# Kernel tuning notes

Hardware: AMD Instinct MI355X
Metric: run time of the kernel (lower is better)

The kernel has to match this reference:

```python
import jax, jax.numpy as jnp
import numpy as np

# ---- constants from the source module ----
NB = [[0,1,2,3],[0,1,4],[0,2,5],[0,3,6],[1,4,7],[2,5,8],[3,6,9],[4,7,10],[5,8,11],[6,9],[7,10],[8,11],[12,13,14,15],[12,13,16],[12,14,17],[12,15],[13,16,18],[14,17,19],[16,18,20],[17,19,21],[18,20,22],[19,21,23],[20,22],[21,23]]
PARENT = np.array([0,0,0,0,1,2,3,4,5,6,7,8,9,9,9,12,13,14,16,17,18,19,20,21])  # root parent sentinel handled separately
KJ, NV, PREG = 24, 6890, 200
LEN = np.array([len(n) for n in NB])
NBR_IDX = np.zeros((KJ,4), np.int32)
NBR_VALID = np.zeros((KJ,4), np.float32)
for k, n in enumerate(NB):
    NBR_IDX[k,:len(n)] = n; NBR_VALID[k,:len(n)] = 1.0
BETA_POS = np.zeros((KJ,17), np.float32); BETA_POS[np.arange(KJ), 4*LEN] = 1.0
SLICE_MASK = np.zeros((23,17), np.float32)
for j in range(23):
    SLICE_MASK[j,:4*LEN[j]+1] = 1.0  # self.K[j] has 4*len(NB[j])+1 rows
NBR_IDX = jnp.asarray(NBR_IDX); NBR_VALID = jnp.asarray(NBR_VALID)
BETA_POS = jnp.asarray(BETA_POS); SLICE_MASK = jnpp = jnp.asarray(SLICE_MASK)


def setup_inputs() -> dict:
    key = jax.random.key(0)
    ks = jax.random.split(key, 9)
    V = jax.random.normal(ks[0], (PREG, NV, 3), jnp.float32)
    T = jax.random.normal(ks[1], (PREG, NV, 3), jnp.float32)
    J = jax.random.normal(ks[2], (PREG, KJ, 3), jnp.float32)
    theta = 0.3 * jax.random.normal(ks[3], (PREG, 72), jnp.float32)
    W_prime = jax.random.uniform(ks[4], (NV, KJ), jnp.float32)
    W_i = jax.random.uniform(ks[5], (NV, KJ), jnp.float32)
    W_i = W_i / W_i.sum(axis=1, keepdims=True)
    A = jax.random.uniform(ks[6], (23, NV), jnp.float32)
    K_mats = 0.01 * jax.random.normal(ks[7], (23, 17, 3 * NV), jnp.float32)
    K_mats = K_mats * SLICE_MASK[:, :, None]  # zero rows beyond the ragged per-joint size
    beta_2 = jnp.ones((1,), jnp.float32)
    return {"V": V, "T": T, "J": J, "theta": theta, "W_prime": W_prime, "W_i": W_i, "A": A, "K_mats": K_mats, "beta_2": beta_2, "epoch": 1}


def _rodrigues(pose):  # pose: (K,3)
    angle = jnp.maximum(jnp.linalg.norm(pose, axis=1, keepdims=True), 1e-8)
    axis = pose / angle
    x, y, z = axis[:, 0], axis[:, 1], axis[:, 2]
    zero = jnp.zeros_like(x)
    skew = jnp.stack([zero, -z, y, z, zero, -x, -y, x, zero], axis=1).reshape(-1, 3, 3)
    outer = axis[:, :, None] * axis[:, None, :]
    c = jnp.cos(angle)[:, :, None]
    s = jnp.sin(angle)[:, :, None]
    eye = jnp.eye(3, dtype=pose.dtype)[None]
    return c * eye + (1.0 - c) * outer + s * skew


def _compute_G(pose72, Jp):  # pose72: (72,), Jp: (K,3) -> (K,4,4)
    R = _rodrigues(pose72.reshape(KJ, 3))
    t = Jp - jnp.concatenate([jnp.zeros((1, 3), Jp.dtype), Jp[PARENT[1:]]], axis=0)
    G_local = jnp.zeros((KJ, 4, 4), Jp.dtype)
    G_local = G_local.at[:, :3, :3].set(R).at[:, :3, 3].set(t).at[:, 3, 3].set(1.0)
    Gs = [G_local[0]]
    for i in range(1, KJ):  # fixed 24-joint kinematic tree
        Gs.append(Gs[PARENT[i]] @ G_local[i])
    G = jnp.stack(Gs, axis=0)
    off = jnp.einsum('kij,kj->ki', G[:, :3, :3], Jp)  # homogeneous w=0 -> rotation only
    return G.at[:, :3, 3].add(-off)


def _axis2quat(p):  # (M,3) -> (M,4)
    angle = jnp.sqrt(jnp.maximum(jnp.sum(p ** 2, axis=1), 1e-16))
    n = p / angle[:, None]
    s = jnp.sin(angle / 2)
    return jnp.stack([n[:, 0] * s, n[:, 1] * s, n[:, 2] * s, jnp.cos(angle / 2) - 1.0], axis=1)


def reference(V, T, J, theta, W_prime, W_i, A, K_mats, beta_2, epoch):
    P = V.shape[0]
    b2 = beta_2[0]
    # normalized skinning weights
    W_relu = jax.nn.relu(W_prime)
    W_change = W_relu / (W_relu.sum(axis=1, keepdims=True) + 1e-8)
    # per-pose global joint transforms
    G_prime = jax.vmap(_compute_G)(theta, J)  # (P,K,4,4)
    # quaternion features and blend-shape correction
    q = _axis2quat(theta.reshape(P * KJ, 3)).reshape(P, KJ, 4)
    qg = q[:, NBR_IDX, :] * NBR_VALID[None, :, :, None]       # (P,K,4,4) neighbor gather
    q17 = jnp.concatenate([qg.reshape(P, KJ, 16), jnp.zeros((P, KJ, 1), q.dtype)], axis=-1)
    q17 = q17 + BETA_POS[None] * b2                            # beta_2 at column 4*len
    qm = q17[:, 1:, :] * SLICE_MASK[None]                      # ragged slice q_ne[:, j+1, :lenK]
    contrib = jnp.einsum('pjl,jlm->pjm', qm, K_mats).reshape(P, 23, NV, 3)
    T_p = jnp.einsum('pjnc,jn->pnc', contrib, jax.nn.relu(A)) + T
    # linear blend skinning
    T_h = jnp.concatenate([T_p, jnp.ones((P, NV, 1), T_p.dtype)], axis=-1)
    transformed = jnp.einsum('pkij,pnj->pnki', G_prime[:, :, :3, :], T_h)  # (P,N,K,3)
    verts = jnp.einsum('nk,pnkc->pnc', W_change, transformed)
    # energies
    e = float(epoch)
    g_wi = 0.1 * np.exp(-0.1 * e)
    g_w = 0.002 * np.exp(-0.008 * e)
    g_a = 0.001 * np.exp(-0.008 * e)
    g_k = 0.1 * np.exp(-0.008 * e)
    E_D = jnp.sum((V - verts) ** 2)
    E_Wi = jnp.sum((W_change - W_i) ** 2)
    E_W = jnp.sum(jnp.abs(W_change))
    E_A = jnp.sum(jnp.abs(A))
    E_K = jnp.sum(jnp.sqrt(jnp.sum(K_mats ** 2, axis=(1, 2))))
    E = E_D + g_wi * E_Wi + g_w * E_W + g_a * E_A + g_k * E_K
    return (E, verts)
```

## Files before the change

kernel.cpp:

```cpp
#include <hip/hip_runtime.h>
#include <math.h>

#define KJ 24
#define NV 6890
#define PREG 200
#define M_TOT (NV*3)
#define KDIM 391
#define KPAD 416
#define TP_STRIDE 20672
#define NMT64 323
#define NKB (NMT64*2)

#define EDP_OFF 0
#define EKP_OFF 5400
#define WIP_OFF 101984
#define EWP_OFF 102016
#define EAP_OFF 102048
#define RED_OFF 102080
#define G_OFF   102112
#define TPH_OFF_U  319424
#define TP2H_OFF_U 4453824
#define QBH_OFF_U 10903488
#define QBL_OFF_U 11009984

typedef __attribute__((ext_vector_type(8))) short short8;
typedef __attribute__((ext_vector_type(4))) float f32x4;
typedef __attribute__((ext_vector_type(4))) unsigned int u32x4;

__constant__ int c_PARENT[24] = {0,0,0,0,1,2,3,4,5,6,7,8,9,9,9,12,13,14,16,17,18,19,20,21};
__constant__ int c_DEPTH[24]  = {0,1,1,1,2,2,2,3,3,3,4,4,4,4,4,5,5,5,6,6,7,7,8,8};
__constant__ int c_LEN[24]    = {4,3,3,3,3,3,3,3,3,2,2,2,4,3,3,2,3,3,3,3,3,3,2,2};
__constant__ int c_NBR[24][4] = {
  {0,1,2,3},{0,1,4,0},{0,2,5,0},{0,3,6,0},{1,4,7,0},{2,5,8,0},{3,6,9,0},{4,7,10,0},
  {5,8,11,0},{6,9,0,0},{7,10,0,0},{8,11,0,0},{12,13,14,15},{12,13,16,0},{12,14,17,0},
  {12,15,0,0},{13,16,18,0},{14,17,19,0},{16,18,20,0},{17,19,21,0},{18,20,22,0},
  {19,21,23,0},{20,22,0,0},{21,23,0,0}};

__device__ __forceinline__ float waveReduce(float v) {
  #pragma unroll
  for (int off = 32; off > 0; off >>= 1) v += __shfl_down(v, off, 64);
  return v;
}
__device__ __forceinline__ unsigned short f2bf(float x) {
  union { float f; unsigned u; } v; v.f = x;
  unsigned r = v.u + 0x7FFFu + ((v.u >> 16) & 1u);
  return (unsigned short)(r >> 16);
}
__device__ __forceinline__ float bf2f(unsigned short h) {
  union { unsigned u; float f; } v; v.u = ((unsigned)h) << 16; return v.f;
}

__global__ __launch_bounds__(256) void kPre(const float* __restrict__ J,
                                            const float* __restrict__ theta,
                                            const float* __restrict__ beta2,
                                            const float* __restrict__ Wp,
                                            const float* __restrict__ Wi,
                                            const float* __restrict__ A,
                                            float* __restrict__ ws) {
  unsigned short* qbh = (unsigned short*)ws + QBH_OFF_U;
  unsigned short* qbl = (unsigned short*)ws + QBL_OFF_U;
  int b = blockIdx.x;
  if (b < 50) {
    __shared__ float Gl[4][24][12];
    __shared__ float Gg[4][24][12];
    __shared__ float q[4][24][4];
    int w = threadIdx.x >> 6, t = threadIdx.x & 63;
    int p = b*4 + w;
    if (t < 24) {
      float x = theta[p*72 + 3*t + 0];
      float y = theta[p*72 + 3*t + 1];
      float z = theta[p*72 + 3*t + 2];
      float n2 = x*x + y*y + z*z;
      float ang = fmaxf(sqrtf(n2), 1e-8f);
      float ia = 1.f/ang;
      float ax = x*ia, ay = y*ia, az = z*ia;
      float c = cosf(ang), s = sinf(ang), C = 1.f - c;
      float jx = J[p*72+3*t], jy = J[p*72+3*t+1], jz = J[p*72+3*t+2];
      float tx = jx, ty = jy, tz = jz;
      if (t > 0) {
        int par = c_PARENT[t];
        tx -= J[p*72+3*par]; ty -= J[p*72+3*par+1]; tz -= J[p*72+3*par+2];
      }
      Gl[w][t][0]=c+C*ax*ax;   Gl[w][t][1]=C*ax*ay-s*az; Gl[w][t][2]=C*ax*az+s*ay; Gl[w][t][3]=tx;
      Gl[w][t][4]=C*ax*ay+s*az;Gl[w][t][5]=c+C*ay*ay;    Gl[w][t][6]=C*ay*az-s*ax; Gl[w][t][7]=ty;
      Gl[w][t][8]=C*ax*az-s*ay;Gl[w][t][9]=C*ay*az+s*ax; Gl[w][t][10]=c+C*az*az;   Gl[w][t][11]=tz;
      float ang2 = sqrtf(fmaxf(n2, 1e-16f));
      float inv2 = 1.f/ang2;
      float s2 = sinf(0.5f*ang2);
      q[w][t][0] = x*inv2*s2; q[w][t][1] = y*inv2*s2; q[w][t][2] = z*inv2*s2;
      q[w][t][3] = cosf(0.5f*ang2) - 1.f;
    }
    __syncthreads();
    for (int lev = 0; lev <= 8; lev++) {
      if (t < 24 && c_DEPTH[t] == lev) {
        if (lev == 0) {
          for (int i2 = 0; i2 < 12; i2++) Gg[w][0][i2] = Gl[w][0][i2];
        } else {
          int par = c_PARENT[t];
          for (int r = 0; r < 3; r++) {
            float g0 = Gg[w][par][r*4+0], g1 = Gg[w][par][r*4+1];
            float g2 = Gg[w][par][r*4+2], g3 = Gg[w][par][r*4+3];
            for (int c2 = 0; c2 < 4; c2++) {
              float v = g0*Gl[w][t][0+c2] + g1*Gl[w][t][4+c2] + g2*Gl[w][t][8+c2];
              if (c2 == 3) v += g3;
              Gg[w][t][r*4+c2] = v;
            }
          }
        }
      }
      __syncthreads();
    }
    if (t < 24) {
      float jx = J[p*72+3*t], jy = J[p*72+3*t+1], jz = J[p*72+3*t+2];
      float* gp = ws + G_OFF + p*288 + t*12;
      #pragma unroll
      for (int r = 0; r < 3; r++) {
        float off = Gg[w][t][r*4+0]*jx + Gg[w][t][r*4+1]*jy + Gg[w][t][r*4+2]*jz;
        Gg[w][t][r*4+3] -= off;
      }
      #pragma unroll
      for (int i2 = 0; i2 < 12; i2++) gp[i2] = Gg[w][t][i2];
    }
    __syncthreads();
    float b2 = beta2[0];
    for (int e = t; e < KDIM; e += 64) {
      int j = e / 17, l = e - 17*j;
      int k = j + 1;
      float val = 0.f;
      if (l < 4*c_LEN[j] + 1) {
        if (l < 16) {
          int sidx = l >> 2, cc = l & 3;
          if (sidx < c_LEN[k]) val = q[w][c_NBR[k][sidx]][cc];
        }
        if (l == 4*c_LEN[k]) val += b2;
      }
      unsigned short hi = f2bf(val);
      unsigned short lo = f2bf(val - bf2f(hi));
      qbh[p*KPAD + e] = hi;
      qbl[p*KPAD + e] = lo;
    }
    for (int e = KDIM + t; e < KPAD; e += 64) {
      qbh[p*KPAD + e] = 0; qbl[p*KPAD + e] = 0;
    }
  } else {
    int d = b - 50;
    int t = threadIdx.x;
    int n = d*256 + t;
    float ewi = 0.f, ew = 0.f, ea = 0.f;
    if (n < NV) {
      float wv[24]; float sum = 0.f;
      const float4* wp4 = (const float4*)(Wp + n*24);
      #pragma unroll
      for (int i = 0; i < 6; i++) {
        float4 v4 = wp4[i];
        wv[4*i+0] = fmaxf(v4.x, 0.f); wv[4*i+1] = fmaxf(v4.y, 0.f);
        wv[4*i+2] = fmaxf(v4.z, 0.f); wv[4*i+3] = fmaxf(v4.w, 0.f);
        sum += wv[4*i+0]+wv[4*i+1]+wv[4*i+2]+wv[4*i+3];
      }
      float inv = 1.f/(sum + 1e-8f);
      #pragma unroll
      for (int k = 0; k < 24; k++) {
        float wc = wv[k]*inv;
        ew += fabsf(wc);
        float dd = wc - Wi[n*24+k];
        ewi += dd*dd;
      }
    }
    for (int i = d*256 + t; i < 23*NV; i += 27*256) ea += fabsf(A[i]);
    for (int i = d*256 + t; i < 56*KPAD; i += 27*256) {
      qbh[200*KPAD + i] = 0; qbl[200*KPAD + i] = 0;
    }
    __shared__ float red[3][4];
    int lane = t & 63, wv2 = t >> 6;
    ewi = waveReduce(ewi); ew = waveReduce(ew); ea = waveReduce(ea);
    if (lane == 0) { red[0][wv2] = ewi; red[1][wv2] = ew; red[2][wv2] = ea; }
    __syncthreads();
    if (t == 0) {
      ws[WIP_OFF + d] = red[0][0]+red[0][1]+red[0][2]+red[0][3];
      ws[EWP_OFF + d] = red[1][0]+red[1][1]+red[1][2]+red[1][3];
      ws[EAP_OFF + d] = red[2][0]+red[2][1]+red[2][2]+red[2][3];
    }
  }
}

template<int KS0, int NKS, int JMIN>
__device__ __forceinline__ void kb_body(const float* __restrict__ A,
                                        const float* __restrict__ K,
                                        const unsigned short* __restrict__ qbh,
                                        const unsigned short* __restrict__ qbl,
                                        float* __restrict__ Sk,
                                        short (*__restrict__ SBh)[64*32],
                                        short (*__restrict__ SBl)[64*32],
                                        float (*__restrict__ SA)[24],
                                        float* __restrict__ ek,
                                        float* __restrict__ ws,
                                        unsigned short* __restrict__ TPd,
                                        int m0, int flat) {
  const int tid = threadIdx.x;
  const int w = tid >> 6, lane = tid & 63;
  const int r = lane & 15, qd = lane >> 4;
  const int krow = tid >> 3, mseg = (tid & 7) * 8;
  const int mm = m0 + mseg;
  const int nb0 = m0 / 3;
  const int mrow2 = tid >> 2, kq2 = tid & 3;
  const int swr = ((mrow2 >> 4)*64 + kq2*16 + (mrow2 & 15)) * 8;

  if (tid < 23) ek[tid] = 0.f;
  for (int i = tid; i < 14*24; i += 256) {
    int jj = i / 24, nn = i - jj*24;
    int j2 = JMIN + jj, n2 = nb0 + nn;
    ((float*)SA)[i] = (j2 < 23 && n2 < NV) ? fmaxf(A[j2*NV + n2], 0.f) : 0.f;
  }

  f32x4 acc[4][4];
  #pragma unroll
  for (int h = 0; h < 4; h++)
    #pragma unroll
    for (int f = 0; f < 4; f++) acc[h][f] = (f32x4){0.f,0.f,0.f,0.f};

  int aofs[4];
  #pragma unroll
  for (int h = 0; h < 4; h++) aofs[h] = (w*64 + h*16 + r)*KPAD + KS0*32 + qd*8;

  short8 ah[2][4], al[2][4];
  float kv[8];

  auto loadK = [&](int ks) {
    int kg = (KS0 + ks)*32 + krow;
    #pragma unroll
    for (int i = 0; i < 8; i++) kv[i] = 0.f;
    if (kg < KDIM) {
      const float* kr = K + (size_t)kg*M_TOT + mm;
      if (mm + 7 < M_TOT) {
        float4 a4 = *(const float4*)kr; float4 b4 = *(const float4*)(kr+4);
        kv[0]=a4.x; kv[1]=a4.y; kv[2]=a4.z; kv[3]=a4.w;
        kv[4]=b4.x; kv[5]=b4.y; kv[6]=b4.z; kv[7]=b4.w;
      } else {
        #pragma unroll
        for (int i = 0; i < 8; i++) if (mm+i < M_TOT) kv[i] = kr[i];
      }
    }
  };
  auto stageK = [&](int ks) {
    int kg = (KS0 + ks)*32 + krow;
    float wv[8]; float sq = 0.f;
    #pragma unroll
    for (int i = 0; i < 8; i++) wv[i] = 0.f;
    if (kg < KDIM) {
      int jj = kg/17 - JMIN;
      int nb = mm / 3;
      float av[4];
      #pragma unroll
      for (int i = 0; i < 4; i++) av[i] = SA[jj][nb - nb0 + i];
      #pragma unroll
      for (int i = 0; i < 8; i++) {
        float a = (mm+i < M_TOT) ? av[(mm+i)/3 - nb] : 0.f;
        wv[i] = kv[i]*a;
        sq = fmaf(kv[i], kv[i], sq);
      }
    }
    #pragma unroll
    for (int c = 0; c < 4; c++)
      *(float2*)&Sk[krow*66 + mseg + 2*c] = make_float2(wv[2*c], wv[2*c+1]);
    sq += __shfl_xor(sq, 1, 64);
    sq += __shfl_xor(sq, 2, 64);
    sq += __shfl_xor(sq, 4, 64);
    if ((tid & 7) == 0 && kg < KDIM) atomicAdd(&ek[kg/17], sq);
  };
  auto xpose = [&](int buf) {
    float vv[8];
    #pragma unroll
    for (int j = 0; j < 8; j++) vv[j] = Sk[(kq2*8 + j)*66 + mrow2];
    unsigned dh[4], dl[4];
    #pragma unroll
    for (int c = 0; c < 4; c++) {
      unsigned short h0 = f2bf(vv[2*c]),   h1 = f2bf(vv[2*c+1]);
      unsigned short l0 = f2bf(vv[2*c]   - bf2f(h0));
      unsigned short l1 = f2bf(vv[2*c+1] - bf2f(h1));
      dh[c] = (unsigned)h0 | ((unsigned)h1 << 16);
      dl[c] = (unsigned)l0 | ((unsigned)l1 << 16);
    }
    *(u32x4*)&SBh[buf][swr] = (u32x4){dh[0], dh[1], dh[2], dh[3]};
    *(u32x4*)&SBl[buf][swr] = (u32x4){dl[0], dl[1], dl[2], dl[3]};
  };

  loadK(0);
  #pragma unroll
  for (int h = 0; h < 4; h++) {
    ah[0][h] = *(const short8*)(qbh + aofs[h]);
    al[0][h] = *(const short8*)(qbl + aofs[h]);
  }
  stageK(0);
  __syncthreads();
  xpose(0);
  #pragma unroll
  for (int h = 0; h < 4; h++) {
    ah[1][h] = *(const short8*)(qbh + aofs[h] + 32);
    al[1][h] = *(const short8*)(qbl + aofs[h] + 32);
  }
  __syncthreads();

  #pragma unroll
  for (int ks = 0; ks < NKS; ks++) {
    const int cur = ks & 1, nxt = cur ^ 1;
    if (ks + 1 < NKS) loadK(ks + 1);
    short8 bfh[4], bfl[4];
    #pragma unroll
    for (int f = 0; f < 4; f++) {
      bfh[f] = *(const short8*)&SBh[cur][(f*64 + lane)*8];
      bfl[f] = *(const short8*)&SBl[cur][(f*64 + lane)*8];
    }
    #pragma unroll
    for (int f = 0; f < 4; f++)
      #pragma unroll
      for (int h = 0; h < 4; h++) {
        acc[h][f] = __builtin_amdgcn_mfma_f32_16x16x32_bf16(ah[cur][h], bfh[f], acc[h][f], 0, 0, 0);
        acc[h][f] = __builtin_amdgcn_mfma_f32_16x16x32_bf16(ah[cur][h], bfl[f], acc[h][f], 0, 0, 0);
        acc[h][f] = __builtin_amdgcn_mfma_f32_16x16x32_bf16(al[cur][h], bfh[f], acc[h][f], 0, 0, 0);
      }
    if (ks + 1 < NKS) stageK(ks + 1);
    if (ks + 2 < NKS) {
      const int o = (ks + 2) * 32;
      #pragma unroll
      for (int h = 0; h < 4; h++) {
        ah[cur][h] = *(const short8*)(qbh + aofs[h] + o);
        al[cur][h] = *(const short8*)(qbl + aofs[h] + o);
      }
    }
    __syncthreads();
    if (ks + 1 < NKS) xpose(nxt);
    __syncthreads();
  }

  if (tid < 23) ws[EKP_OFF + tid*NKB + flat] = ek[tid];
  #pragma unroll
  for (int h = 0; h < 4; h++)
    #pragma unroll
    for (int f = 0; f < 4; f++)
      #pragma unroll
      for (int g = 0; g < 4; g++) {
        int p = w*64 + h*16 + qd*4 + g;
        if (p < PREG)
          TPd[(size_t)p*TP_STRIDE + m0 + f*16 + r] = f2bf(acc[h][f][g]);
      }
}

__global__ __launch_bounds__(256) void kB(const float* __restrict__ A,
                                          const float* __restrict__ K,
                                          float* __restrict__ ws) {
  __shared__ float Sk[32*66];
  __shared__ short SBh[2][64*32];
  __shared__ short SBl[2][64*32];
  __shared__ float SA[14][24];
  __shared__ float ek[23];
  const unsigned short* qbh = (const unsigned short*)ws + QBH_OFF_U;
  const unsigned short* qbl = (const unsigned short*)ws + QBL_OFF_U;
  unsigned short* tph  = (unsigned short*)ws + TPH_OFF_U;
  unsigned short* tp2h = (unsigned short*)ws + TP2H_OFF_U;
  const int m0 = blockIdx.x * 64;
  const int flat = blockIdx.x + blockIdx.y * NMT64;
  if (blockIdx.y == 0)
    kb_body<0, 7, 0>(A, K, qbh, qbl, Sk, SBh, SBl, SA, ek, ws, tph,  m0, flat);
  else
    kb_body<7, 6, 13>(A, K, qbh, qbl, Sk, SBh, SBl, SA, ek, ws, tp2h, m0, flat);
}

__global__ __launch_bounds__(256) void kC(const float* __restrict__ V,
                                          const float* __restrict__ T,
                                          const float* __restrict__ Wp,
                                          const float* __restrict__ ws,
                                          float* __restrict__ out) {
  int p0 = blockIdx.y * 8;
  int n = blockIdx.x*256 + threadIdx.x;
  const unsigned short* tph  = (const unsigned short*)ws + TPH_OFF_U;
  const unsigned short* tp2h = (const unsigned short*)ws + TP2H_OFF_U;
  __shared__ float tmp[4];
  float ed = 0.f;
  if (n < NV) {
    float wv[24]; float sum = 0.f;
    const float4* wp4 = (const float4*)(Wp + n*24);
    #pragma unroll
    for (int i = 0; i < 6; i++) {
      float4 v4 = wp4[i];
      wv[4*i+0] = fmaxf(v4.x, 0.f); wv[4*i+1] = fmaxf(v4.y, 0.f);
      wv[4*i+2] = fmaxf(v4.z, 0.f); wv[4*i+3] = fmaxf(v4.w, 0.f);
      sum += wv[4*i+0]+wv[4*i+1]+wv[4*i+2]+wv[4*i+3];
    }
    float inv = 1.f/(sum + 1e-8f);
    for (int pp = 0; pp < 8; pp++) {
      int p = p0 + pp;
      const float* __restrict__ gp = ws + G_OFF + (size_t)p*288;
      float M[12];
      #pragma unroll
      for (int i = 0; i < 12; i++) M[i] = 0.f;
      #pragma unroll
      for (int k = 0; k < 24; k++) {
        float wc = wv[k];
        #pragma unroll
        for (int i = 0; i < 12; i++)
          M[i] = fmaf(wc, gp[k*12 + i], M[i]);
      }
      #pragma unroll
      for (int i = 0; i < 12; i++) M[i] *= inv;
      size_t tb = (size_t)p*M_TOT + 3*n;
      size_t pb = (size_t)p*TP_STRIDE + 3*n;
      float t0 = bf2f(tph[pb + 0]) + bf2f(tp2h[pb + 0]) + T[tb + 0];
      float t1 = bf2f(tph[pb + 1]) + bf2f(tp2h[pb + 1]) + T[tb + 1];
      float t2 = bf2f(tph[pb + 2]) + bf2f(tp2h[pb + 2]) + T[tb + 2];
      float v0 = M[0]*t0 + M[1]*t1 + M[2]*t2  + M[3];
      float v1 = M[4]*t0 + M[5]*t1 + M[6]*t2  + M[7];
      float v2 = M[8]*t0 + M[9]*t1 + M[10]*t2 + M[11];
      out[1+tb+0] = v0; out[1+tb+1] = v1; out[1+tb+2] = v2;
      float d0 = V[tb+0]-v0, d1 = V[tb+1]-v1, d2 = V[tb+2]-v2;
      ed += d0*d0 + d1*d1 + d2*d2;
    }
  }
  ed = waveReduce(ed);
  int lane = threadIdx.x & 63, w = threadIdx.x >> 6;
  if (lane == 0) tmp[w] = ed;
  __syncthreads();
  if (threadIdx.x == 0)
    ((float*)ws)[EDP_OFF + blockIdx.y*27 + blockIdx.x] = tmp[0]+tmp[1]+tmp[2]+tmp[3];
}

__global__ __launch_bounds__(256) void kF1(float* __restrict__ ws) {
  __shared__ float sb[4];
  int b = blockIdx.x, t = threadIdx.x, lane = t & 63, w = t >> 6;
  if (b < 23) {
    float s = 0.f;
    for (int i = t; i < NKB; i += 256) s += ws[EKP_OFF + b*NKB + i];
    s = waveReduce(s);
    if (lane == 0) sb[w] = s;
    __syncthreads();
    if (t == 0) ws[RED_OFF + b] = sb[0]+sb[1]+sb[2]+sb[3];
  } else if (b == 23) {
    float s = 0.f;
    for (int i = t; i < 675; i += 256) s += ws[EDP_OFF + i];
    s = waveReduce(s);
    if (lane == 0) sb[w] = s;
    __syncthreads();
    if (t == 0) ws[RED_OFF + 23] = sb[0]+sb[1]+sb[2]+sb[3];
  } else {
    if (w == 0) {
      float s = (lane < 27) ? ws[WIP_OFF + lane] : 0.f;
      s = waveReduce(s);
      if (lane == 0) ws[RED_OFF + 24] = s;
    } else if (w == 1) {
      float s = (lane < 27) ? ws[EWP_OFF + lane] : 0.f;
      s = waveReduce(s);
      if (lane == 0) ws[RED_OFF + 25] = s;
    } else if (w == 2) {
      float s = (lane < 27) ? ws[EAP_OFF + lane] : 0.f;
      s = waveReduce(s);
      if (lane == 0) ws[RED_OFF + 26] = s;
    }
  }
}

__global__ void kF2(const int* __restrict__ epoch, const float* __restrict__ ws,
                    float* __restrict__ out) {
  int t = threadIdx.x;
  float s = (t < 23) ? sqrtf(ws[RED_OFF + t]) : 0.f;
  s = waveReduce(s);
  if (t == 0) {
    float e    = (float)epoch[0];
    float g_wi = 0.1f   * expf(-0.1f  * e);
    float g_w  = 0.002f * expf(-0.008f* e);
    float g_a  = 0.001f * expf(-0.008f* e);
    float g_k  = 0.1f   * expf(-0.008f* e);
    out[0] = ws[RED_OFF+23] + g_wi*ws[RED_OFF+24] + g_w*ws[RED_OFF+25]
           + g_a*ws[RED_OFF+26] + g_k*s;
  }
}

extern "C" void kernel_launch(void* const* d_in, const int* in_sizes, int n_in,
                              void* d_out, int out_size, void* d_ws, size_t ws_size,
                              hipStream_t stream) {
  const float* V     = (const float*)d_in[0];
  const float* T     = (const float*)d_in[1];
  const float* J     = (const float*)d_in[2];
  const float* theta = (const float*)d_in[3];
  const float* Wp    = (const float*)d_in[4];
  const float* Wi    = (const float*)d_in[5];
  const float* A     = (const float*)d_in[6];
  const float* K     = (const float*)d_in[7];
  const float* b2    = (const float*)d_in[8];
  const int*   epoch = (const int*)d_in[9];
  float* out = (float*)d_out;
  float* ws  = (float*)d_ws;

  hipLaunchKernelGGL(kPre, dim3(77),        dim3(256), 0, stream,
                     J, theta, b2, Wp, Wi, A, ws);
  hipLaunchKernelGGL(kB,   dim3(NMT64, 2),  dim3(256), 0, stream, A, K, ws);
  hipLaunchKernelGGL(kC,   dim3(27, 25),    dim3(256), 0, stream, V, T, Wp, ws, out);
  hipLaunchKernelGGL(kF1,  dim3(25),        dim3(256), 0, stream, ws);
  hipLaunchKernelGGL(kF2,  dim3(1),         dim3(64),  0, stream, epoch, ws, out);
}
```

Measured before the change: 177.5 us.

## Deepen K-tile software pipeline in kB and drop LDS atomics for E_K

```diff
diff --git a/kernel.cpp b/kernel.cpp
--- a/kernel.cpp
+++ b/kernel.cpp
@@ -188,11 +188,11 @@
                                         const float* __restrict__ K,
                                         const unsigned short* __restrict__ qbh,
                                         const unsigned short* __restrict__ qbl,
-                                        float* __restrict__ Sk,
+                                        float (*__restrict__ Sk)[32*66],
                                         short (*__restrict__ SBh)[64*32],
                                         short (*__restrict__ SBl)[64*32],
                                         float (*__restrict__ SA)[24],
-                                        float* __restrict__ ek,
+                                        float* __restrict__ ek2,
                                         float* __restrict__ ws,
                                         unsigned short* __restrict__ TPd,
                                         int m0, int flat) {
@@ -205,7 +205,6 @@
   const int mrow2 = tid >> 2, kq2 = tid & 3;
   const int swr = ((mrow2 >> 4)*64 + kq2*16 + (mrow2 & 15)) * 8;
 
-  if (tid < 23) ek[tid] = 0.f;
   for (int i = tid; i < 14*24; i += 256) {
     int jj = i / 24, nn = i - jj*24;
     int j2 = JMIN + jj, n2 = nb0 + nn;
@@ -223,76 +222,74 @@
   for (int h = 0; h < 4; h++) aofs[h] = (w*64 + h*16 + r)*KPAD + KS0*32 + qd*8;
 
   short8 ah[2][4], al[2][4];
-  float kv[8];
-
-  auto loadK = [&](int ks) {
-    int kg = (KS0 + ks)*32 + krow;
-    #pragma unroll
-    for (int i = 0; i < 8; i++) kv[i] = 0.f;
-    if (kg < KDIM) {
-      const float* kr = K + (size_t)kg*M_TOT + mm;
-      if (mm + 7 < M_TOT) {
-        float4 a4 = *(const float4*)kr; float4 b4 = *(const float4*)(kr+4);
-        kv[0]=a4.x; kv[1]=a4.y; kv[2]=a4.z; kv[3]=a4.w;
-        kv[4]=b4.x; kv[5]=b4.y; kv[6]=b4.z; kv[7]=b4.w;
-      } else {
-        #pragma unroll
-        for (int i = 0; i < 8; i++) if (mm+i < M_TOT) kv[i] = kr[i];
-      }
-    }
-  };
-  auto stageK = [&](int ks) {
-    int kg = (KS0 + ks)*32 + krow;
-    float wv[8]; float sq = 0.f;
-    #pragma unroll
-    for (int i = 0; i < 8; i++) wv[i] = 0.f;
-    if (kg < KDIM) {
-      int jj = kg/17 - JMIN;
-      int nb = mm / 3;
-      float av[4];
-      #pragma unroll
-      for (int i = 0; i < 4; i++) av[i] = SA[jj][nb - nb0 + i];
-      #pragma unroll
-      for (int i = 0; i < 8; i++) {
-        float a = (mm+i < M_TOT) ? av[(mm+i)/3 - nb] : 0.f;
-        wv[i] = kv[i]*a;
-        sq = fmaf(kv[i], kv[i], sq);
-      }
-    }
-    #pragma unroll
-    for (int c = 0; c < 4; c++)
-      *(float2*)&Sk[krow*66 + mseg + 2*c] = make_float2(wv[2*c], wv[2*c+1]);
-    sq += __shfl_xor(sq, 1, 64);
-    sq += __shfl_xor(sq, 2, 64);
-    sq += __shfl_xor(sq, 4, 64);
-    if ((tid & 7) == 0 && kg < KDIM) atomicAdd(&ek[kg/17], sq);
-  };
-  auto xpose = [&](int buf) {
-    float vv[8];
-    #pragma unroll
-    for (int j = 0; j < 8; j++) vv[j] = Sk[(kq2*8 + j)*66 + mrow2];
-    unsigned dh[4], dl[4];
-    #pragma unroll
-    for (int c = 0; c < 4; c++) {
-      unsigned short h0 = f2bf(vv[2*c]),   h1 = f2bf(vv[2*c+1]);
-      unsigned short l0 = f2bf(vv[2*c]   - bf2f(h0));
-      unsigned short l1 = f2bf(vv[2*c+1] - bf2f(h1));
-      dh[c] = (unsigned)h0 | ((unsigned)h1 << 16);
-      dl[c] = (unsigned)l0 | ((unsigned)l1 << 16);
-    }
-    *(u32x4*)&SBh[buf][swr] = (u32x4){dh[0], dh[1], dh[2], dh[3]};
-    *(u32x4*)&SBl[buf][swr] = (u32x4){dl[0], dl[1], dl[2], dl[3]};
-  };
-
-  loadK(0);
+  float kvA[8], kvB[8];
+
+#define LOADK(KSV, KV) do {                                                    \
+    int kg_ = (KS0 + (KSV))*32 + krow;                                         \
+    for (int i_ = 0; i_ < 8; i_++) KV[i_] = 0.f;                               \
+    if (kg_ < KDIM) {                                                          \
+      const float* kr_ = K + (size_t)kg_*M_TOT + mm;                           \
+      if (mm + 7 < M_TOT) {                                                    \
+        float4 a4_ = *(const float4*)kr_; float4 b4_ = *(const float4*)(kr_+4);\
+        KV[0]=a4_.x; KV[1]=a4_.y; KV[2]=a4_.z; KV[3]=a4_.w;                    \
+        KV[4]=b4_.x; KV[5]=b4_.y; KV[6]=b4_.z; KV[7]=b4_.w;                    \
+      } else {                                                                 \
+        for (int i_ = 0; i_ < 8; i_++) if (mm+i_ < M_TOT) KV[i_] = kr_[i_];    \
+      }                                                                        \
+    } } while (0)
+
+#define STAGEK(KSV, KV) do {                                                   \
+    int kg_ = (KS0 + (KSV))*32 + krow;                                         \
+    float wv_[8]; float sq_ = 0.f;                                             \
+    for (int i_ = 0; i_ < 8; i_++) wv_[i_] = 0.f;                              \
+    if (kg_ < KDIM) {                                                          \
+      int jj_ = kg_/17 - JMIN;                                                 \
+      int nb_ = mm / 3;                                                        \
+      float av_[4];                                                            \
+      for (int i_ = 0; i_ < 4; i_++) av_[i_] = SA[jj_][nb_ - nb0 + i_];        \
+      for (int i_ = 0; i_ < 8; i_++) {                                         \
+        float a_ = (mm+i_ < M_TOT) ? av_[(mm+i_)/3 - nb_] : 0.f;               \
+        wv_[i_] = KV[i_]*a_;                                                   \
+        sq_ = fmaf(KV[i_], KV[i_], sq_);                                       \
+      }                                                                        \
+    }                                                                          \
+    for (int c_ = 0; c_ < 4; c_++)                                             \
+      *(float2*)&Sk[(KSV)&1][krow*66 + mseg + 2*c_] =                          \
+        make_float2(wv_[2*c_], wv_[2*c_+1]);                                   \
+    sq_ += __shfl_xor(sq_, 1, 64);                                             \
+    sq_ += __shfl_xor(sq_, 2, 64);                                             \
+    sq_ += __shfl_xor(sq_, 4, 64);                                             \
+    if ((tid & 7) == 0) ek2[(KSV)*32 + krow] = sq_;                            \
+  } while (0)
+
+#define XPOSE(KSV) do {                                                        \
+    float vv_[8];                                                              \
+    for (int j_ = 0; j_ < 8; j_++)                                             \
+      vv_[j_] = Sk[(KSV)&1][(kq2*8 + j_)*66 + mrow2];                          \
+    unsigned dh_[4], dl_[4];                                                   \
+    for (int c_ = 0; c_ < 4; c_++) {                                           \
+      unsigned short h0_ = f2bf(vv_[2*c_]),   h1_ = f2bf(vv_[2*c_+1]);         \
+      unsigned short l0_ = f2bf(vv_[2*c_]   - bf2f(h0_));                      \
+      unsigned short l1_ = f2bf(vv_[2*c_+1] - bf2f(h1_));                      \
+      dh_[c_] = (unsigned)h0_ | ((unsigned)h1_ << 16);                         \
+      dl_[c_] = (unsigned)l0_ | ((unsigned)l1_ << 16);                         \
+    }                                                                          \
+    *(u32x4*)&SBh[(KSV)&1][swr] = (u32x4){dh_[0], dh_[1], dh_[2], dh_[3]};     \
+    *(u32x4*)&SBl[(KSV)&1][swr] = (u32x4){dl_[0], dl_[1], dl_[2], dl_[3]};     \
+  } while (0)
+
+  LOADK(0, kvA);
   #pragma unroll
   for (int h = 0; h < 4; h++) {
     ah[0][h] = *(const short8*)(qbh + aofs[h]);
     al[0][h] = *(const short8*)(qbl + aofs[h]);
   }
-  stageK(0);
+  STAGEK(0, kvA);
+  LOADK(1, kvB);
   __syncthreads();
-  xpose(0);
+  XPOSE(0);
+  STAGEK(1, kvB);
+  LOADK(2, kvA);
   #pragma unroll
   for (int h = 0; h < 4; h++) {
     ah[1][h] = *(const short8*)(qbh + aofs[h] + 32);
@@ -302,8 +299,10 @@
 
   #pragma unroll
   for (int ks = 0; ks < NKS; ks++) {
-    const int cur = ks & 1, nxt = cur ^ 1;
-    if (ks + 1 < NKS) loadK(ks + 1);
+    const int cur = ks & 1;
+    if (ks + 3 < NKS) {
+      if (cur == 1) LOADK(ks + 3, kvA); else LOADK(ks + 3, kvB);
+    }
     short8 bfh[4], bfl[4];
     #pragma unroll
     for (int f = 0; f < 4; f++) {
@@ -318,7 +317,6 @@
         acc[h][f] = __builtin_amdgcn_mfma_f32_16x16x32_bf16(ah[cur][h], bfl[f], acc[h][f], 0, 0, 0);
         acc[h][f] = __builtin_amdgcn_mfma_f32_16x16x32_bf16(al[cur][h], bfh[f], acc[h][f], 0, 0, 0);
       }
-    if (ks + 1 < NKS) stageK(ks + 1);
     if (ks + 2 < NKS) {
       const int o = (ks + 2) * 32;
       #pragma unroll
@@ -327,12 +325,24 @@
         al[cur][h] = *(const short8*)(qbl + aofs[h] + o);
       }
     }
+    if (ks + 2 < NKS) {
+      if (cur == 0) STAGEK(ks + 2, kvA); else STAGEK(ks + 2, kvB);
+    }
+    if (ks + 1 < NKS) XPOSE(ks + 1);
     __syncthreads();
-    if (ks + 1 < NKS) xpose(nxt);
-    __syncthreads();
-  }
-
-  if (tid < 23) ws[EKP_OFF + tid*NKB + flat] = ek[tid];
+  }
+#undef LOADK
+#undef STAGEK
+#undef XPOSE
+
+  if (tid < 23) {
+    float s = 0.f;
+    for (int i2 = 0; i2 < NKS*32; i2++) {
+      int kg = KS0*32 + i2;
+      if (kg < KDIM && kg/17 == tid) s += ek2[i2];
+    }
+    ws[EKP_OFF + tid*NKB + flat] = s;
+  }
   #pragma unroll
   for (int h = 0; h < 4; h++)
     #pragma unroll
@@ -348,11 +358,11 @@
 __global__ __launch_bounds__(256) void kB(const float* __restrict__ A,
                                           const float* __restrict__ K,
                                           float* __restrict__ ws) {
-  __shared__ float Sk[32*66];
+  __shared__ float Sk[2][32*66];
   __shared__ short SBh[2][64*32];
   __shared__ short SBl[2][64*32];
   __shared__ float SA[14][24];
-  __shared__ float ek[23];
+  __shared__ float ek2[7*32];
   const unsigned short* qbh = (const unsigned short*)ws + QBH_OFF_U;
   const unsigned short* qbl = (const unsigned short*)ws + QBL_OFF_U;
   unsigned short* tph  = (unsigned short*)ws + TPH_OFF_U;
@@ -360,9 +370,9 @@
   const int m0 = blockIdx.x * 64;
   const int flat = blockIdx.x + blockIdx.y * NMT64;
   if (blockIdx.y == 0)
-    kb_body<0, 7, 0>(A, K, qbh, qbl, Sk, SBh, SBl, SA, ek, ws, tph,  m0, flat);
+    kb_body<0, 7, 0>(A, K, qbh, qbl, Sk, SBh, SBl, SA, ek2, ws, tph,  m0, flat);
   else
-    kb_body<7, 6, 13>(A, K, qbh, qbl, Sk, SBh, SBl, SA, ek, ws, tp2h, m0, flat);
+    kb_body<7, 6, 13>(A, K, qbh, qbl, Sk, SBh, SBl, SA, ek2, ws, tp2h, m0, flat);
 }
 
 __global__ __launch_bounds__(256) void kC(const float* __restrict__ V,
```

Measured after the change: 186.3 us. +5.0%, slower.

## Split K-projection GEMM four ways and move K-norm energy into prologue

Applied to the files above, without the earlier changes.

```diff
diff --git a/kernel.cpp b/kernel.cpp
--- a/kernel.cpp
+++ b/kernel.cpp
@@ -9,7 +9,6 @@
 #define KPAD 416
 #define TP_STRIDE 20672
 #define NMT64 323
-#define NKB (NMT64*2)
 
 #define EDP_OFF 0
 #define EKP_OFF 5400
@@ -18,10 +17,13 @@
 #define EAP_OFF 102048
 #define RED_OFF 102080
 #define G_OFF   102112
+#define TPQ_U   4134400
 #define TPH_OFF_U  319424
-#define TP2H_OFF_U 4453824
-#define QBH_OFF_U 10903488
-#define QBL_OFF_U 11009984
+#define TP2H_OFF_U (TPH_OFF_U + TPQ_U)
+#define TP3H_OFF_U (TPH_OFF_U + 2*TPQ_U)
+#define TP4H_OFF_U (TPH_OFF_U + 3*TPQ_U)
+#define QBH_OFF_U  16857024
+#define QBL_OFF_U  16963520
 
 typedef __attribute__((ext_vector_type(8))) short short8;
 typedef __attribute__((ext_vector_type(4))) float f32x4;
@@ -56,6 +58,7 @@
                                             const float* __restrict__ Wp,
                                             const float* __restrict__ Wi,
                                             const float* __restrict__ A,
+                                            const float* __restrict__ K,
                                             float* __restrict__ ws) {
   unsigned short* qbh = (unsigned short*)ws + QBH_OFF_U;
   unsigned short* qbl = (unsigned short*)ws + QBL_OFF_U;
@@ -142,7 +145,7 @@
     for (int e = KDIM + t; e < KPAD; e += 64) {
       qbh[p*KPAD + e] = 0; qbl[p*KPAD + e] = 0;
     }
-  } else {
+  } else if (b < 77) {
     int d = b - 50;
     int t = threadIdx.x;
     int n = d*256 + t;
@@ -180,6 +183,18 @@
       ws[EWP_OFF + d] = red[1][0]+red[1][1]+red[1][2]+red[1][3];
       ws[EAP_OFF + d] = red[2][0]+red[2][1]+red[2][2]+red[2][3];
     }
+  } else {
+    int kg = b - 77;
+    int t = threadIdx.x;
+    const float* kr = K + (size_t)kg*M_TOT;
+    float s = 0.f;
+    for (int i = t; i < M_TOT; i += 256) { float v = kr[i]; s = fmaf(v, v, s); }
+    __shared__ float sb[4];
+    int lane = t & 63, w = t >> 6;
+    s = waveReduce(s);
+    if (lane == 0) sb[w] = s;
+    __syncthreads();
+    if (t == 0) ws[EKP_OFF + kg] = sb[0]+sb[1]+sb[2]+sb[3];
   }
 }
 
@@ -192,10 +207,8 @@
                                         short (*__restrict__ SBh)[64*32],
                                         short (*__restrict__ SBl)[64*32],
                                         float (*__restrict__ SA)[24],
-                                        float* __restrict__ ek,
-                                        float* __restrict__ ws,
                                         unsigned short* __restrict__ TPd,
-                                        int m0, int flat) {
+                                        int m0) {
   const int tid = threadIdx.x;
   const int w = tid >> 6, lane = tid & 63;
   const int r = lane & 15, qd = lane >> 4;
@@ -205,7 +218,6 @@
   const int mrow2 = tid >> 2, kq2 = tid & 3;
   const int swr = ((mrow2 >> 4)*64 + kq2*16 + (mrow2 & 15)) * 8;
 
-  if (tid < 23) ek[tid] = 0.f;
   for (int i = tid; i < 14*24; i += 256) {
     int jj = i / 24, nn = i - jj*24;
     int j2 = JMIN + jj, n2 = nb0 + nn;
@@ -243,7 +255,7 @@
   };
   auto stageK = [&](int ks) {
     int kg = (KS0 + ks)*32 + krow;
-    float wv[8]; float sq = 0.f;
+    float wv[8];
     #pragma unroll
     for (int i = 0; i < 8; i++) wv[i] = 0.f;
     if (kg < KDIM) {
@@ -256,16 +268,11 @@
       for (int i = 0; i < 8; i++) {
         float a = (mm+i < M_TOT) ? av[(mm+i)/3 - nb] : 0.f;
         wv[i] = kv[i]*a;
-        sq = fmaf(kv[i], kv[i], sq);
       }
     }
     #pragma unroll
     for (int c = 0; c < 4; c++)
       *(float2*)&Sk[krow*66 + mseg + 2*c] = make_float2(wv[2*c], wv[2*c+1]);
-    sq += __shfl_xor(sq, 1, 64);
-    sq += __shfl_xor(sq, 2, 64);
-    sq += __shfl_xor(sq, 4, 64);
-    if ((tid & 7) == 0 && kg < KDIM) atomicAdd(&ek[kg/17], sq);
   };
   auto xpose = [&](int buf) {
     float vv[8];
@@ -332,7 +339,6 @@
     __syncthreads();
   }
 
-  if (tid < 23) ws[EKP_OFF + tid*NKB + flat] = ek[tid];
   #pragma unroll
   for (int h = 0; h < 4; h++)
     #pragma unroll
@@ -352,17 +358,17 @@
   __shared__ short SBh[2][64*32];
   __shared__ short SBl[2][64*32];
   __shared__ float SA[14][24];
-  __shared__ float ek[23];
   const unsigned short* qbh = (const unsigned short*)ws + QBH_OFF_U;
   const unsigned short* qbl = (const unsigned short*)ws + QBL_OFF_U;
-  unsigned short* tph  = (unsigned short*)ws + TPH_OFF_U;
-  unsigned short* tp2h = (unsigned short*)ws + TP2H_OFF_U;
   const int m0 = blockIdx.x * 64;
-  const int flat = blockIdx.x + blockIdx.y * NMT64;
   if (blockIdx.y == 0)
-    kb_body<0, 7, 0>(A, K, qbh, qbl, Sk, SBh, SBl, SA, ek, ws, tph,  m0, flat);
+    kb_body<0, 4, 0>(A, K, qbh, qbl, Sk, SBh, SBl, SA, (unsigned short*)ws + TPH_OFF_U,  m0);
+  else if (blockIdx.y == 1)
+    kb_body<4, 3, 7>(A, K, qbh, qbl, Sk, SBh, SBl, SA, (unsigned short*)ws + TP2H_OFF_U, m0);
+  else if (blockIdx.y == 2)
+    kb_body<7, 3, 13>(A, K, qbh, qbl, Sk, SBh, SBl, SA, (unsigned short*)ws + TP3H_OFF_U, m0);
   else
-    kb_body<7, 6, 13>(A, K, qbh, qbl, Sk, SBh, SBl, SA, ek, ws, tp2h, m0, flat);
+    kb_body<10, 3, 18>(A, K, qbh, qbl, Sk, SBh, SBl, SA, (unsigned short*)ws + TP4H_OFF_U, m0);
 }
 
 __global__ __launch_bounds__(256) void kC(const float* __restrict__ V,
@@ -372,8 +378,10 @@
                                           float* __restrict__ out) {
   int p0 = blockIdx.y * 8;
   int n = blockIdx.x*256 + threadIdx.x;
-  const unsigned short* tph  = (const unsigned short*)ws + TPH_OFF_U;
-  const unsigned short* tp2h = (const unsigned short*)ws + TP2H_OFF_U;
+  const unsigned short* tp1 = (const unsigned short*)ws + TPH_OFF_U;
+  const unsigned short* tp2 = (const unsigned short*)ws + TP2H_OFF_U;
+  const unsigned short* tp3 = (const unsigned short*)ws + TP3H_OFF_U;
+  const unsigned short* tp4 = (const unsigned short*)ws + TP4H_OFF_U;
   __shared__ float tmp[4];
   float ed = 0.f;
   if (n < NV) {
@@ -404,9 +412,9 @@
       for (int i = 0; i < 12; i++) M[i] *= inv;
       size_t tb = (size_t)p*M_TOT + 3*n;
       size_t pb = (size_t)p*TP_STRIDE + 3*n;
-      float t0 = bf2f(tph[pb + 0]) + bf2f(tp2h[pb + 0]) + T[tb + 0];
-      float t1 = bf2f(tph[pb + 1]) + bf2f(tp2h[pb + 1]) + T[tb + 1];
-      float t2 = bf2f(tph[pb + 2]) + bf2f(tp2h[pb + 2]) + T[tb + 2];
+      float t0 = bf2f(tp1[pb+0]) + bf2f(tp2[pb+0]) + bf2f(tp3[pb+0]) + bf2f(tp4[pb+0]) + T[tb + 0];
+      float t1 = bf2f(tp1[pb+1]) + bf2f(tp2[pb+1]) + bf2f(tp3[pb+1]) + bf2f(tp4[pb+1]) + T[tb + 1];
+      float t2 = bf2f(tp1[pb+2]) + bf2f(tp2[pb+2]) + bf2f(tp3[pb+2]) + bf2f(tp4[pb+2]) + T[tb + 2];
       float v0 = M[0]*t0 + M[1]*t1 + M[2]*t2  + M[3];
       float v1 = M[4]*t0 + M[5]*t1 + M[6]*t2  + M[7];
       float v2 = M[8]*t0 + M[9]*t1 + M[10]*t2 + M[11];
@@ -427,12 +435,11 @@
   __shared__ float sb[4];
   int b = blockIdx.x, t = threadIdx.x, lane = t & 63, w = t >> 6;
   if (b < 23) {
-    float s = 0.f;
-    for (int i = t; i < NKB; i += 256) s += ws[EKP_OFF + b*NKB + i];
-    s = waveReduce(s);
-    if (lane == 0) sb[w] = s;
-    __syncthreads();
-    if (t == 0) ws[RED_OFF + b] = sb[0]+sb[1]+sb[2]+sb[3];
+    if (w == 0) {
+      float s = (lane < 17) ? ws[EKP_OFF + b*17 + lane] : 0.f;
+      s = waveReduce(s);
+      if (lane == 0) ws[RED_OFF + b] = s;
+    }
   } else if (b == 23) {
     float s = 0.f;
     for (int i = t; i < 675; i += 256) s += ws[EDP_OFF + i];
@@ -489,9 +496,9 @@
   float* out = (float*)d_out;
   float* ws  = (float*)d_ws;
 
-  hipLaunchKernelGGL(kPre, dim3(77),        dim3(256), 0, stream,
-                     J, theta, b2, Wp, Wi, A, ws);
-  hipLaunchKernelGGL(kB,   dim3(NMT64, 2),  dim3(256), 0, stream, A, K, ws);
+  hipLaunchKernelGGL(kPre, dim3(77 + KDIM), dim3(256), 0, stream,
+                     J, theta, b2, Wp, Wi, A, K, ws);
+  hipLaunchKernelGGL(kB,   dim3(NMT64, 4),  dim3(256), 0, stream, A, K, ws);
   hipLaunchKernelGGL(kC,   dim3(27, 25),    dim3(256), 0, stream, V, T, Wp, ws, out);
   hipLaunchKernelGGL(kF1,  dim3(25),        dim3(256), 0, stream, ws);
   hipLaunchKernelGGL(kF2,  dim3(1),         dim3(64),  0, stream, epoch, ws, out);
```

Measured after the change: 197.7 us. 1.11x slower.
